# Kernel optimization log

Measured on AMD Instinct MI355X. Metric: run time of the kernel, lower is better.

Reference implementation:

```python
import jax, jax.numpy as jnp
import numpy as np

B, L, M, H = 4096, 512, 17, 17  # batch, seq_len, num_features, latent_dim


def setup_inputs() -> dict:
    key = jax.random.key(0)
    ks = jax.random.split(key, 5)
    s = 1.0 / np.sqrt(H)  # torch nn.LSTM init scale
    x = jax.random.normal(ks[0], (B, L, M), dtype=jnp.float32)
    W_ih = jax.random.uniform(ks[1], (4 * H, M), dtype=jnp.float32, minval=-s, maxval=s)
    W_hh = jax.random.uniform(ks[2], (4 * H, H), dtype=jnp.float32, minval=-s, maxval=s)
    b_ih = jax.random.uniform(ks[3], (4 * H,), dtype=jnp.float32, minval=-s, maxval=s)
    b_hh = jax.random.uniform(ks[4], (4 * H,), dtype=jnp.float32, minval=-s, maxval=s)
    return {"x": x, "W_ih": W_ih, "W_hh": W_hh, "b_ih": b_ih, "b_hh": b_hh}


def _lstm(x, W_ih, W_hh, b_ih, b_hh):
    # Precompute input projections for all timesteps in one GEMM: (B,L,4H)
    xW = jnp.einsum('blm,gm->blg', x, W_ih) + b_ih + b_hh
    xW_t = jnp.swapaxes(xW, 0, 1)  # (L,B,4H) for scan over time
    W_hh_T = W_hh.T  # (H,4H)

    def step(carry, xw_t):
        h, c = carry
        gates = xw_t + h @ W_hh_T  # (B,4H)
        i, f, g, o = jnp.split(gates, 4, axis=-1)  # torch gate order: i,f,g,o
        i = jax.nn.sigmoid(i)
        f = jax.nn.sigmoid(f)
        g = jnp.tanh(g)
        o = jax.nn.sigmoid(o)
        c_new = f * c + i * g
        h_new = o * jnp.tanh(c_new)
        return (h_new, c_new), h_new

    h0 = jnp.zeros((x.shape[0], W_hh.shape[1]), dtype=x.dtype)
    c0 = jnp.zeros_like(h0)
    (h_f, c_f), hs = jax.lax.scan(step, (h0, c0), xW_t)
    out = jnp.swapaxes(hs, 0, 1)  # (B,L,H)
    return out, h_f, c_f


def reference(x, W_ih, W_hh, b_ih, b_hh):
    out, h_f, c_f = _lstm(x, W_ih, W_hh, b_ih, b_hh)
    # match torch return: out, (h,c) with leading num_layers dim, and x
    return out, (h_f[None], c_f[None]), x
```

## Files before the change

kernel.cpp:

```cpp
#include <hip/hip_runtime.h>
#include <hip/hip_bf16.h>


namespace {
constexpr int B_TOT = 4096;
constexpr int L_SEQ = 512;
constexpr int NF    = 17;
constexpr int BS    = 16;
constexpr int TPB   = 320;
constexpr int TC    = 16;
constexpr int NCHUNK = L_SEQ / TC;
constexpr int KPAD  = 24;
constexpr int F4_PER_ROW   = TC * NF / 4;
constexpr int F4_PER_CHUNK = BS * F4_PER_ROW;
constexpr int PF_MAX = (F4_PER_CHUNK + TPB - 1) / TPB;

constexpr int OUT_H = B_TOT * L_SEQ * NF;
constexpr int OUT_C = OUT_H + B_TOT * NF;
constexpr int OUT_X = OUT_C + B_TOT * NF;
}

typedef __attribute__((ext_vector_type(8))) short bf16x8;
typedef __attribute__((ext_vector_type(4))) float f32x4;

__device__ __forceinline__ unsigned short f2bf(float f) {
  union { float f; unsigned int u; } v; v.f = f;
  unsigned int r = v.u + 0x7fff + ((v.u >> 16) & 1);
  return (unsigned short)(r >> 16);
}
__device__ __forceinline__ unsigned short h2bf(float f) {
  unsigned int r;
  asm("v_cvt_pk_bf16_f32 %0, %1, %2" : "=v"(r) : "v"(f), "v"(f));
  return (unsigned short)r;
}
__device__ __forceinline__ float sigm(float x) {
  return __builtin_amdgcn_rcpf(1.f + __expf(-x));
}
__device__ __forceinline__ float tanh_fast(float x) {
  float e = __expf(2.f * x);
  return 1.f - 2.f * __builtin_amdgcn_rcpf(e + 1.f);
}

__device__ __forceinline__ void gstore1(float* p, float v) {
  asm volatile("global_store_dword %0, %1, off" :: "v"(p), "v"(v));
}
__device__ __forceinline__ void gstore4(float* p, f32x4 v) {
  asm volatile("global_store_dwordx4 %0, %1, off" :: "v"(p), "v"(v));
}

__device__ __forceinline__ void block_sync_lds() {
  asm volatile("s_waitcnt lgkmcnt(0)" ::: "memory");
  __builtin_amdgcn_s_barrier();
  asm volatile("" ::: "memory");
}

__global__ void __launch_bounds__(TPB) lstm_kernel(
    const float* __restrict__ x, const float* __restrict__ W_ih,
    const float* __restrict__ W_hh, const float* __restrict__ b_ih,
    const float* __restrict__ b_hh, float* __restrict__ out)
{
  __shared__ __align__(16) unsigned short x_s[2][TC][BS][KPAD];
  __shared__ __align__(16) unsigned short h_s[2][BS][KPAD];
  __shared__ __align__(16) unsigned short w0_s[80][32];
  __shared__ __align__(16) unsigned short w1_s[80][32];
  __shared__ __align__(16) float bias_s[80];
  __shared__ __align__(16) unsigned short zero16[8];

  const int tid  = threadIdx.x;
  const int lane = tid & 63;
  const int T    = tid >> 6;
  const int bb   = lane & 15;
  const int q    = lane >> 4;
  const int b0   = blockIdx.x * BS;

  f32x4 pf[PF_MAX];
  #pragma unroll
  for (int i = 0; i < PF_MAX; ++i) {
    int u = tid + TPB * i;
    if (u < F4_PER_CHUNK) {
      int row = u / F4_PER_ROW, off = u % F4_PER_ROW;
      pf[i] = *(const f32x4*)(x + ((b0 + row) * L_SEQ) * NF + off * 4);
    }
  }

  {
    unsigned int* p = (unsigned int*)&x_s[0][0][0][0];
    for (int u = tid; u < (int)(sizeof(x_s) / 4); u += TPB) p[u] = 0;
    unsigned int* ph = (unsigned int*)&h_s[0][0][0];
    for (int u = tid; u < (int)(sizeof(h_s) / 4); u += TPB) ph[u] = 0;
    if (tid < 4) ((unsigned int*)zero16)[tid] = 0;
  }
  for (int u = tid; u < 80 * 32; u += TPB) {
    int r = u >> 5, k = u & 31;
    unsigned short v0 = 0, v1 = 0;
    int j = -1, ty = 0;
    if (r < 64)      { j = r >> 2; ty = r & 3; }
    else if (r < 68) { j = 16;     ty = r - 64; }
    if (j >= 0 && k < NF) {
      int g = ty * NF + j;
      v0 = f2bf(W_ih[g * NF + k]);
      v1 = f2bf(W_hh[g * NF + k]);
    }
    w0_s[r][k] = v0; w1_s[r][k] = v1;
  }
  for (int u = tid; u < 80; u += TPB) {
    float bv = 0.f; int j = -1, ty = 0;
    if (u < 64)      { j = u >> 2; ty = u & 3; }
    else if (u < 68) { j = 16;     ty = u - 64; }
    if (j >= 0) { int g = ty * NF + j; bv = b_ih[g] + b_hh[g]; }
    bias_s[u] = bv;
  }
  __syncthreads();

  auto stage = [&](int cn) {
    #pragma unroll
    for (int i = 0; i < PF_MAX; ++i) {
      int u = tid + TPB * i;
      if (u < F4_PER_CHUNK) {
        int row = u / F4_PER_ROW, off = u % F4_PER_ROW;
        int gidx = ((b0 + row) * L_SEQ + cn * TC) * NF + off * 4;
        gstore4(out + OUT_X + gidx, pf[i]);
        int p = off * 4, tl = p / NF, m = p - tl * NF;
        #pragma unroll
        for (int e = 0; e < 4; ++e) {
          x_s[cn & 1][tl][row][m] = f2bf(pf[i][e]);
          if (++m == NF) { m = 0; ++tl; }
        }
      }
    }
  };
  auto prefetch = [&](int cn) {
    #pragma unroll
    for (int i = 0; i < PF_MAX; ++i) {
      int u = tid + TPB * i;
      if (u < F4_PER_CHUNK) {
        int row = u / F4_PER_ROW, off = u % F4_PER_ROW;
        pf[i] = *(const f32x4*)(x + ((b0 + row) * L_SEQ + cn * TC) * NF + off * 4);
      }
    }
  };

  stage(0);
  prefetch(1);

  const bf16x8 a0 = *(const bf16x8*)&w0_s[16 * T + bb][q * 8];
  const bf16x8 a1 = *(const bf16x8*)&w1_s[16 * T + bb][q * 8];
  const f32x4 bias4 = *(const f32x4*)&bias_s[16 * T + q * 4];

  const int j = 4 * T + q;
  const bool active = (T < 4) || (q == 0);
  const int jj = (j > 16) ? 16 : j;

  const unsigned short* const xbase0 = (q == 3) ? zero16 : &x_s[0][0][bb][q * 8];
  const unsigned short* const xbase1 = (q == 3) ? zero16 : &x_s[1][0][bb][q * 8];
  const int xstep = (q == 3) ? 0 : BS * KPAD;
  const unsigned short* const hr0 = (q == 3) ? zero16 : &h_s[0][bb][q * 8];
  const unsigned short* const hr1 = (q == 3) ? zero16 : &h_s[1][bb][q * 8];
  unsigned short* const hw0 = &h_s[1][bb][jj];
  unsigned short* const hw1 = &h_s[0][bb][jj];

  float c_st = 0.f, h_last = 0.f;
  float* outp = out + (b0 + bb) * L_SEQ * NF + jj;

  auto epilogue = [&](const f32x4& acc, unsigned short* hwp) {
    if (active) {
      float gi = sigm(acc[0]);
      float gf = sigm(acc[1]);
      float gg = tanh_fast(acc[2]);
      float go = sigm(acc[3]);
      c_st   = gf * c_st + gi * gg;
      h_last = go * tanh_fast(c_st);
      *hwp = h2bf(h_last);
      gstore1(outp, h_last);
      outp += NF;
    }
  };

  for (int c = 0; c < NCHUNK; ++c) {
    block_sync_lds();

    const unsigned short* xq = (c & 1) ? xbase1 : xbase0;
    f32x4 hist[TC];
    #pragma unroll
    for (int tt = 0; tt < TC; ++tt) {
      bf16x8 bx = *(const bf16x8*)(xq + tt * xstep);
      hist[tt] = __builtin_amdgcn_mfma_f32_16x16x32_bf16(a0, bx, bias4, 0, 0, 0);
    }

    #pragma unroll
    for (int tt = 0; tt < TC; tt += 2) {
      block_sync_lds();
      {
        bf16x8 bh = *(const bf16x8*)hr0;
        f32x4 acc = __builtin_amdgcn_mfma_f32_16x16x32_bf16(a1, bh, hist[tt], 0, 0, 0);
        epilogue(acc, hw0);
      }
      block_sync_lds();
      {
        bf16x8 bh = *(const bf16x8*)hr1;
        f32x4 acc = __builtin_amdgcn_mfma_f32_16x16x32_bf16(a1, bh, hist[tt + 1], 0, 0, 0);
        epilogue(acc, hw1);
      }
    }

    if (c + 1 < NCHUNK) {
      stage(c + 1);
      if (c + 2 < NCHUNK) prefetch(c + 2);
    }
  }

  if (active) {
    gstore1(out + OUT_H + (b0 + bb) * NF + j, h_last);
    gstore1(out + OUT_C + (b0 + bb) * NF + j, c_st);
  }
}

extern "C" void kernel_launch(void* const* d_in, const int* in_sizes, int n_in,
                              void* d_out, int out_size, void* d_ws, size_t ws_size,
                              hipStream_t stream) {
  (void)in_sizes; (void)n_in; (void)out_size; (void)d_ws; (void)ws_size;
  const float* x    = (const float*)d_in[0];
  const float* W_ih = (const float*)d_in[1];
  const float* W_hh = (const float*)d_in[2];
  const float* b_ih = (const float*)d_in[3];
  const float* b_hh = (const float*)d_in[4];
  float* out = (float*)d_out;
  hipLaunchKernelGGL(lstm_kernel, dim3(B_TOT / BS), dim3(TPB), 0, stream,
                     x, W_ih, W_hh, b_ih, b_hh, out);
}
```

Measured before the change: 454.7 us.

## Drop fifth wavefront by computing hidden unit 16 redundantly in all four waves

Reduces the block from five wavefronts to four. Each wave now also computes the MFMA and gate nonlinearities for hidden unit 16 redundantly, and only wave 0 stores its output while lane group q0 writes its h value to LDS. This cuts the per-step barrier participants and removes a mostly idle wave that held only one active lane group. In exchange every wave does twice the MFMA and transcendental work on the serial recurrence path, and register pressure rises from the extra hist4 array.

```diff
diff --git a/kernel.cpp b/kernel.cpp
--- a/kernel.cpp
+++ b/kernel.cpp
@@ -7,7 +7,7 @@
 constexpr int L_SEQ = 512;
 constexpr int NF    = 17;
 constexpr int BS    = 16;
-constexpr int TPB   = 320;
+constexpr int TPB   = 256;
 constexpr int TC    = 16;
 constexpr int NCHUNK = L_SEQ / TC;
 constexpr int KPAD  = 24;
@@ -54,7 +54,7 @@
   asm volatile("" ::: "memory");
 }
 
-__global__ void __launch_bounds__(TPB) lstm_kernel(
+__global__ void __launch_bounds__(TPB, 1) lstm_kernel(
     const float* __restrict__ x, const float* __restrict__ W_ih,
     const float* __restrict__ W_hh, const float* __restrict__ b_ih,
     const float* __restrict__ b_hh, float* __restrict__ out)
@@ -143,48 +143,42 @@
   stage(0);
   prefetch(1);
 
-  const bf16x8 a0 = *(const bf16x8*)&w0_s[16 * T + bb][q * 8];
-  const bf16x8 a1 = *(const bf16x8*)&w1_s[16 * T + bb][q * 8];
-  const f32x4 bias4 = *(const f32x4*)&bias_s[16 * T + q * 4];
+  const bf16x8 a0  = *(const bf16x8*)&w0_s[16 * T + bb][q * 8];
+  const bf16x8 a1  = *(const bf16x8*)&w1_s[16 * T + bb][q * 8];
+  const f32x4 bias4  = *(const f32x4*)&bias_s[16 * T + q * 4];
+  const bf16x8 a40 = *(const bf16x8*)&w0_s[64 + bb][q * 8];
+  const bf16x8 a41 = *(const bf16x8*)&w1_s[64 + bb][q * 8];
+  const f32x4 bias44 = *(const f32x4*)&bias_s[64 + q * 4];
 
   const int j = 4 * T + q;
-  const bool active = (T < 4) || (q == 0);
-  const int jj = (j > 16) ? 16 : j;
+  const bool q0   = (q == 0);
+  const bool w0q0 = (T == 0) && q0;
 
   const unsigned short* const xbase0 = (q == 3) ? zero16 : &x_s[0][0][bb][q * 8];
   const unsigned short* const xbase1 = (q == 3) ? zero16 : &x_s[1][0][bb][q * 8];
   const int xstep = (q == 3) ? 0 : BS * KPAD;
   const unsigned short* const hr0 = (q == 3) ? zero16 : &h_s[0][bb][q * 8];
   const unsigned short* const hr1 = (q == 3) ? zero16 : &h_s[1][bb][q * 8];
-  unsigned short* const hw0 = &h_s[1][bb][jj];
-  unsigned short* const hw1 = &h_s[0][bb][jj];
-
-  float c_st = 0.f, h_last = 0.f;
-  float* outp = out + (b0 + bb) * L_SEQ * NF + jj;
-
-  auto epilogue = [&](const f32x4& acc, unsigned short* hwp) {
-    if (active) {
-      float gi = sigm(acc[0]);
-      float gf = sigm(acc[1]);
-      float gg = tanh_fast(acc[2]);
-      float go = sigm(acc[3]);
-      c_st   = gf * c_st + gi * gg;
-      h_last = go * tanh_fast(c_st);
-      *hwp = h2bf(h_last);
-      gstore1(outp, h_last);
-      outp += NF;
-    }
-  };
+  unsigned short* const hwA0 = &h_s[1][bb][j];
+  unsigned short* const hwA1 = &h_s[0][bb][j];
+  unsigned short* const hw40 = &h_s[1][bb][16];
+  unsigned short* const hw41 = &h_s[0][bb][16];
+
+  float cA = 0.f, hA = 0.f;
+  float c4 = 0.f, h4 = 0.f;
+  float* outpA = out + (b0 + bb) * L_SEQ * NF + j;
+  float* outp4 = out + (b0 + bb) * L_SEQ * NF + 16;
 
   for (int c = 0; c < NCHUNK; ++c) {
     block_sync_lds();
 
     const unsigned short* xq = (c & 1) ? xbase1 : xbase0;
-    f32x4 hist[TC];
+    f32x4 hist[TC], hist4[TC];
     #pragma unroll
     for (int tt = 0; tt < TC; ++tt) {
       bf16x8 bx = *(const bf16x8*)(xq + tt * xstep);
-      hist[tt] = __builtin_amdgcn_mfma_f32_16x16x32_bf16(a0, bx, bias4, 0, 0, 0);
+      hist [tt] = __builtin_amdgcn_mfma_f32_16x16x32_bf16(a0,  bx, bias4,  0, 0, 0);
+      hist4[tt] = __builtin_amdgcn_mfma_f32_16x16x32_bf16(a40, bx, bias44, 0, 0, 0);
     }
 
     #pragma unroll
@@ -192,14 +186,48 @@
       block_sync_lds();
       {
         bf16x8 bh = *(const bf16x8*)hr0;
-        f32x4 acc = __builtin_amdgcn_mfma_f32_16x16x32_bf16(a1, bh, hist[tt], 0, 0, 0);
-        epilogue(acc, hw0);
+        f32x4 accA = __builtin_amdgcn_mfma_f32_16x16x32_bf16(a1,  bh, hist [tt], 0, 0, 0);
+        f32x4 acc4 = __builtin_amdgcn_mfma_f32_16x16x32_bf16(a41, bh, hist4[tt], 0, 0, 0);
+        {
+          float gi = sigm(accA[0]), gf = sigm(accA[1]);
+          float gg = tanh_fast(accA[2]), go = sigm(accA[3]);
+          cA = gf * cA + gi * gg;
+          hA = go * tanh_fast(cA);
+          *hwA0 = h2bf(hA);
+          gstore1(outpA, hA); outpA += NF;
+        }
+        {
+          float gi = sigm(acc4[0]), gf = sigm(acc4[1]);
+          float gg = tanh_fast(acc4[2]), go = sigm(acc4[3]);
+          c4 = gf * c4 + gi * gg;
+          h4 = go * tanh_fast(c4);
+          if (q0)   *hw40 = h2bf(h4);
+          if (w0q0) gstore1(outp4, h4);
+          outp4 += NF;
+        }
       }
       block_sync_lds();
       {
         bf16x8 bh = *(const bf16x8*)hr1;
-        f32x4 acc = __builtin_amdgcn_mfma_f32_16x16x32_bf16(a1, bh, hist[tt + 1], 0, 0, 0);
-        epilogue(acc, hw1);
+        f32x4 accA = __builtin_amdgcn_mfma_f32_16x16x32_bf16(a1,  bh, hist [tt + 1], 0, 0, 0);
+        f32x4 acc4 = __builtin_amdgcn_mfma_f32_16x16x32_bf16(a41, bh, hist4[tt + 1], 0, 0, 0);
+        {
+          float gi = sigm(accA[0]), gf = sigm(accA[1]);
+          float gg = tanh_fast(accA[2]), go = sigm(accA[3]);
+          cA = gf * cA + gi * gg;
+          hA = go * tanh_fast(cA);
+          *hwA1 = h2bf(hA);
+          gstore1(outpA, hA); outpA += NF;
+        }
+        {
+          float gi = sigm(acc4[0]), gf = sigm(acc4[1]);
+          float gg = tanh_fast(acc4[2]), go = sigm(acc4[3]);
+          c4 = gf * c4 + gi * gg;
+          h4 = go * tanh_fast(c4);
+          if (q0)   *hw41 = h2bf(h4);
+          if (w0q0) gstore1(outp4, h4);
+          outp4 += NF;
+        }
       }
     }
 
@@ -209,9 +237,11 @@
     }
   }
 
-  if (active) {
-    gstore1(out + OUT_H + (b0 + bb) * NF + j, h_last);
-    gstore1(out + OUT_C + (b0 + bb) * NF + j, c_st);
+  gstore1(out + OUT_H + (b0 + bb) * NF + j, hA);
+  gstore1(out + OUT_C + (b0 + bb) * NF + j, cA);
+  if (w0q0) {
+    gstore1(out + OUT_H + (b0 + bb) * NF + 16, h4);
+    gstore1(out + OUT_C + (b0 + bb) * NF + 16, c4);
   }
 }
 
```

New measurement: 476.0 us. 4.7% more time.
